# Performance work log

Hardware: AMD Instinct MI355X
Metric: run time of the kernel (lower is better)

The kernel has to match this reference:

```python
import jax, jax.numpy as jnp
import numpy as np

# constants from __init__ defaults
K_WINNERS = 5
GAIN_UP = 1.8
MIN_GAIN = 0.5
MAX_GAIN = 2.5
THETA = 1.0

B, T = 512, 8192


def setup_inputs() -> dict:
    key = jax.random.key(0)
    k1, k2, k3 = jax.random.split(key, 3)
    amp = jax.random.uniform(k1, (B, T), jnp.float32)
    pitch = jax.random.uniform(k2, (B, T), jnp.float32)
    boundary = jax.random.uniform(k3, (B, T), jnp.float32)
    decay = jnp.array([0.7, 0.7, 0.7], jnp.float32)    # buffer 'decay'
    weights = jnp.array([1.0, 1.0, 1.0], jnp.float32)  # buffer 'weights'
    return {"amp": amp, "pitch": pitch, "boundary": boundary,
            "decay": decay, "weights": weights}


def reference(amp, pitch, boundary, decay, weights):
    # Stack the 3 channels so one scan handles all LIF neurons: xs [3, B, T]
    xs = jnp.stack([amp, pitch, boundary], axis=0)
    d = decay[:, None]  # [3, 1] broadcast over batch

    def step(v, x_t):          # v, x_t: [3, B]
        v = d * v + x_t
        s = (v >= THETA).astype(v.dtype)
        return v - s * THETA, s

    v0 = jnp.zeros((3, B), xs.dtype)
    _, spikes = jax.lax.scan(step, v0, jnp.moveaxis(xs, 2, 0))  # spikes [T, 3, B]

    # salience = w_amp*s_amp + w_pitch*s_pitch + w_bound*s_bound -> [B, T]
    sal = jnp.einsum('c,tcb->bt', weights, spikes)
    # smoothing == 0 -> conv branch skipped (matches default init)
    sal = sal / (jnp.max(sal, axis=1, keepdims=True) + 1e-6)

    topk_vals, topk_idx = jax.lax.top_k(sal, K_WINNERS)  # [B, K]
    avg_winner = topk_vals.mean(axis=1)                  # [B]
    mu_scalar = MIN_GAIN + (MAX_GAIN - MIN_GAIN) * jnp.tanh(GAIN_UP * avg_winner)
    return mu_scalar, sal, topk_idx
```

## Files before the change

kernel.cpp:

```cpp
#include <hip/hip_runtime.h>
#include <cstdint>
#include <cstddef>

#define BB 512
#define TT 8192
#define TW 256
#define KWIN 5

static __device__ __forceinline__ float fract_f(float x) {
#if __has_builtin(__builtin_amdgcn_fractf)
    return __builtin_amdgcn_fractf(x);
#else
    return x - floorf(x);
#endif
}

__global__ __launch_bounds__(64, 2)
void lif_scan_kernel(const float* __restrict__ amp,
                     const float* __restrict__ pitch,
                     const float* __restrict__ boundary,
                     const float* __restrict__ decay,
                     float* __restrict__ out)
{
    const int blk = blockIdx.x;
    const int c   = blk >> 9;
    const int b   = blk & 511;
    const int l   = threadIdx.x;
    const float* __restrict__ src =
        (c == 0 ? amp : (c == 1 ? pitch : boundary)) + (size_t)b * TT;
    const float dv = decay[c];

    const float4* __restrict__ w4 = reinterpret_cast<const float4*>(src) + 32 * l;
    float4 W[32];
#pragma unroll
    for (int i = 0; i < 32; ++i) W[i] = w4[i];

    float v = 0.0f;

    const bool z = (l == 0);
#define WSTEP(xx)                                               \
    {                                                           \
        float xw = __shfl_up((xx), 1);                          \
        if (z) xw = 0.0f;                                       \
        float t2 = __fadd_rn(__fmul_rn(dv, v), xw);             \
        v = fract_f(t2);                                        \
    }
#pragma unroll
    for (int i = 0; i < 32; ++i) {
        WSTEP(W[i].x) WSTEP(W[i].y) WSTEP(W[i].z) WSTEP(W[i].w)
    }
#undef WSTEP

    uint32_t w[4];
    float bs;
#define KSTEP(xx)                                               \
    {                                                           \
        float t2 = __fadd_rn(__fmul_rn(dv, v), (xx));           \
        float nv = fract_f(t2);                                 \
        bs = __builtin_fmaf(2.0f, bs, t2 - nv);                 \
        v = nv;                                                 \
    }
#pragma unroll
    for (int q = 0; q < 4; ++q) {
        bs = 0.0f;
#pragma unroll
        for (int i = 8 * q; i < 8 * q + 4; ++i) {
            KSTEP(W[i].x) KSTEP(W[i].y) KSTEP(W[i].z) KSTEP(W[i].w)
        }
        const uint32_t hi = (uint32_t)bs;
        bs = 0.0f;
#pragma unroll
        for (int i = 8 * q + 4; i < 8 * q + 8; ++i) {
            KSTEP(W[i].x) KSTEP(W[i].y) KSTEP(W[i].z) KSTEP(W[i].w)
        }
        w[q] = (hi << 16) | (uint32_t)bs;
    }
#undef KSTEP

    uint32_t* wout = reinterpret_cast<uint32_t*>(out + 512 + (size_t)b * TT)
                   + c * TW;
    *reinterpret_cast<uint4*>(wout + 4 * l) = make_uint4(w[0], w[1], w[2], w[3]);
}

__global__ __launch_bounds__(256, 2)
void salience_topk_kernel(const float* __restrict__ weights,
                          float* __restrict__ out)
{
    const int b = blockIdx.x;
    const int tid = threadIdx.x;

    __shared__ uint32_t words[3 * TW];
    __shared__ uint32_t spres[4];
    __shared__ float ntab[8];
    __shared__ uint32_t htab[8];
    __shared__ unsigned long long red[4];
    __shared__ unsigned long long wins;

    float* sal_out = out + 512 + (size_t)b * TT;
    const uint32_t* wsrc = reinterpret_cast<const uint32_t*>(sal_out);

    words[tid]       = wsrc[tid];
    words[tid + 256] = wsrc[tid + 256];
    words[tid + 512] = wsrc[tid + 512];

    const float w0 = weights[0], w1 = weights[1], w2 = weights[2];
    __syncthreads();

    uint32_t pres = 0;
#pragma unroll
    for (int j = 0; j < 8; ++j) {
        const int t0 = 4 * tid + 1024 * j;
        const int wi = t0 >> 5;
        const uint32_t wa = words[wi], wp = words[TW + wi], wq = words[2 * TW + wi];
#pragma unroll
        for (int k = 0; k < 4; ++k) {
            const int sh = 31 - ((t0 & 31) + k);
            const uint32_t idx = ((wa >> sh) & 1u)
                               | (((wp >> sh) & 1u) << 1)
                               | (((wq >> sh) & 1u) << 2);
            pres |= (1u << idx);
        }
    }
#pragma unroll
    for (int off = 32; off; off >>= 1)
        pres |= __shfl_down(pres, off);
    if ((tid & 63) == 0) spres[tid >> 6] = pres;
    __syncthreads();

    if (tid < 8) {
        const uint32_t p = spres[0] | spres[1] | spres[2] | spres[3];
        float s0 = (float)(tid & 1), s1 = (float)((tid >> 1) & 1), s2 = (float)(tid >> 2);
        float tv = __fadd_rn(__fadd_rn(__fmul_rn(w0, s0), __fmul_rn(w1, s1)),
                             __fmul_rn(w2, s2));
        float m = ((p >> tid) & 1u) ? tv : -INFINITY;
        m = fmaxf(m, __shfl_xor(m, 1));
        m = fmaxf(m, __shfl_xor(m, 2));
        m = fmaxf(m, __shfl_xor(m, 4));
        const float denom = __fadd_rn(m, 1e-6f);
        float nv = tv / denom;
        ntab[tid] = nv;
        uint32_t ub = __float_as_uint(nv);
        htab[tid] = (ub & 0x80000000u) ? ~ub : (ub | 0x80000000u);
    }
    __syncthreads();

    unsigned long long t5[5] = {0ull, 0ull, 0ull, 0ull, 0ull};
#pragma unroll
    for (int j = 0; j < 8; ++j) {
        const int t0 = 4 * tid + 1024 * j;
        const int wi = t0 >> 5;
        const uint32_t wa = words[wi], wp = words[TW + wi], wq = words[2 * TW + wi];
        float4 q;
        float* qp = &q.x;
#pragma unroll
        for (int k = 0; k < 4; ++k) {
            const int sh = 31 - ((t0 & 31) + k);
            const uint32_t idx = ((wa >> sh) & 1u)
                               | (((wp >> sh) & 1u) << 1)
                               | (((wq >> sh) & 1u) << 2);
            qp[k] = ntab[idx];
            unsigned long long key = ((unsigned long long)htab[idx] << 32)
                                   | (unsigned long long)(uint32_t)(TT - 1 - (t0 + k));
            if (key > t5[4]) {
#pragma unroll
                for (int i = 0; i < 5; ++i) {
                    bool g = key > t5[i];
                    unsigned long long o = t5[i];
                    t5[i] = g ? key : o;
                    key   = g ? o : key;
                }
            }
        }
        *reinterpret_cast<float4*>(sal_out + t0) = q;
    }

    float vsum = 0.0f;
    for (int r = 0; r < KWIN; ++r) {
        unsigned long long cand = t5[0];
#pragma unroll
        for (int off = 32; off; off >>= 1) {
            unsigned long long o = __shfl_down(cand, off);
            if (o > cand) cand = o;
        }
        __syncthreads();
        if ((tid & 63) == 0) red[tid >> 6] = cand;
        __syncthreads();
        if (tid == 0) {
            unsigned long long m = red[0];
            if (red[1] > m) m = red[1];
            if (red[2] > m) m = red[2];
            if (red[3] > m) m = red[3];
            wins = m;
        }
        __syncthreads();
        const unsigned long long w = wins;
        if (t5[0] == w) {
            t5[0] = t5[1]; t5[1] = t5[2]; t5[2] = t5[3]; t5[3] = t5[4]; t5[4] = 0ull;
        }
        if (tid == 0) {
            uint32_t hi = (uint32_t)(w >> 32);
            uint32_t fb = (hi & 0x80000000u) ? (hi & 0x7FFFFFFFu) : ~hi;
            vsum += __uint_as_float(fb);
            out[512 + (size_t)BB * TT + (size_t)b * KWIN + r] =
                (float)(int)(TT - 1 - (uint32_t)(w & 0xFFFFFFFFull));
        }
    }

    if (tid == 0) {
        out[b] = 0.5f + 2.0f * tanhf(1.8f * (vsum / 5.0f));
    }
}

extern "C" void kernel_launch(void* const* d_in, const int* in_sizes, int n_in,
                              void* d_out, int out_size, void* d_ws, size_t ws_size,
                              hipStream_t stream) {
    const float* amp      = (const float*)d_in[0];
    const float* pitch    = (const float*)d_in[1];
    const float* boundary = (const float*)d_in[2];
    const float* decay    = (const float*)d_in[3];
    const float* weights  = (const float*)d_in[4];
    float* out = (float*)d_out;

    lif_scan_kernel<<<3 * BB, 64, 0, stream>>>(amp, pitch, boundary, decay, out);
    salience_topk_kernel<<<BB, 256, 0, stream>>>(weights, out);
}
```

Before: 114.6 us.

## Fuse LIF scan and salience top-k into one kernel via shared-memory bitmasks

Merges the two kernels into one launch. Three of the four waves in each 256-thread block run the per-channel LIF scans and write the spike bitmasks straight into shared memory, so the global round trip through the output buffer and the second launch go away. The cost is that the fourth wave sits idle during the scan. The block now uses 128 float4 registers per scan wave under a 256-thread launch bound, and there are only 512 blocks where the scan stage used to have 1536 blocks, so occupancy and latency hiding may drop.

```diff
diff --git a/kernel.cpp b/kernel.cpp
--- a/kernel.cpp
+++ b/kernel.cpp
@@ -15,79 +15,18 @@
 #endif
 }
 
-__global__ __launch_bounds__(64, 2)
-void lif_scan_kernel(const float* __restrict__ amp,
-                     const float* __restrict__ pitch,
-                     const float* __restrict__ boundary,
-                     const float* __restrict__ decay,
-                     float* __restrict__ out)
+__global__ __launch_bounds__(256, 2)
+void fused_spike_topk_kernel(const float* __restrict__ amp,
+                             const float* __restrict__ pitch,
+                             const float* __restrict__ boundary,
+                             const float* __restrict__ decay,
+                             const float* __restrict__ weights,
+                             float* __restrict__ out)
 {
-    const int blk = blockIdx.x;
-    const int c   = blk >> 9;
-    const int b   = blk & 511;
-    const int l   = threadIdx.x;
-    const float* __restrict__ src =
-        (c == 0 ? amp : (c == 1 ? pitch : boundary)) + (size_t)b * TT;
-    const float dv = decay[c];
-
-    const float4* __restrict__ w4 = reinterpret_cast<const float4*>(src) + 32 * l;
-    float4 W[32];
-#pragma unroll
-    for (int i = 0; i < 32; ++i) W[i] = w4[i];
-
-    float v = 0.0f;
-
-    const bool z = (l == 0);
-#define WSTEP(xx)                                               \
-    {                                                           \
-        float xw = __shfl_up((xx), 1);                          \
-        if (z) xw = 0.0f;                                       \
-        float t2 = __fadd_rn(__fmul_rn(dv, v), xw);             \
-        v = fract_f(t2);                                        \
-    }
-#pragma unroll
-    for (int i = 0; i < 32; ++i) {
-        WSTEP(W[i].x) WSTEP(W[i].y) WSTEP(W[i].z) WSTEP(W[i].w)
-    }
-#undef WSTEP
-
-    uint32_t w[4];
-    float bs;
-#define KSTEP(xx)                                               \
-    {                                                           \
-        float t2 = __fadd_rn(__fmul_rn(dv, v), (xx));           \
-        float nv = fract_f(t2);                                 \
-        bs = __builtin_fmaf(2.0f, bs, t2 - nv);                 \
-        v = nv;                                                 \
-    }
-#pragma unroll
-    for (int q = 0; q < 4; ++q) {
-        bs = 0.0f;
-#pragma unroll
-        for (int i = 8 * q; i < 8 * q + 4; ++i) {
-            KSTEP(W[i].x) KSTEP(W[i].y) KSTEP(W[i].z) KSTEP(W[i].w)
-        }
-        const uint32_t hi = (uint32_t)bs;
-        bs = 0.0f;
-#pragma unroll
-        for (int i = 8 * q + 4; i < 8 * q + 8; ++i) {
-            KSTEP(W[i].x) KSTEP(W[i].y) KSTEP(W[i].z) KSTEP(W[i].w)
-        }
-        w[q] = (hi << 16) | (uint32_t)bs;
-    }
-#undef KSTEP
-
-    uint32_t* wout = reinterpret_cast<uint32_t*>(out + 512 + (size_t)b * TT)
-                   + c * TW;
-    *reinterpret_cast<uint4*>(wout + 4 * l) = make_uint4(w[0], w[1], w[2], w[3]);
-}
-
-__global__ __launch_bounds__(256, 2)
-void salience_topk_kernel(const float* __restrict__ weights,
-                          float* __restrict__ out)
-{
-    const int b = blockIdx.x;
-    const int tid = threadIdx.x;
+    const int b    = blockIdx.x;
+    const int tid  = threadIdx.x;
+    const int wave = tid >> 6;
+    const int l    = tid & 63;
 
     __shared__ uint32_t words[3 * TW];
     __shared__ uint32_t spres[4];
@@ -96,12 +35,63 @@
     __shared__ unsigned long long red[4];
     __shared__ unsigned long long wins;
 
-    float* sal_out = out + 512 + (size_t)b * TT;
-    const uint32_t* wsrc = reinterpret_cast<const uint32_t*>(sal_out);
-
-    words[tid]       = wsrc[tid];
-    words[tid + 256] = wsrc[tid + 256];
-    words[tid + 512] = wsrc[tid + 512];
+    if (wave < 3) {
+        const int c = wave;
+        const float* __restrict__ src =
+            (c == 0 ? amp : (c == 1 ? pitch : boundary)) + (size_t)b * TT;
+        const float dv = decay[c];
+
+        const float4* __restrict__ w4 =
+            reinterpret_cast<const float4*>(src) + 32 * l;
+        float4 W[32];
+#pragma unroll
+        for (int i = 0; i < 32; ++i) W[i] = w4[i];
+
+        float v = 0.0f;
+
+        const bool z = (l == 0);
+#define WSTEP(xx)                                               \
+        {                                                       \
+            float xw = __shfl_up((xx), 1);                      \
+            if (z) xw = 0.0f;                                   \
+            float t2 = __fadd_rn(__fmul_rn(dv, v), xw);         \
+            v = fract_f(t2);                                    \
+        }
+#pragma unroll
+        for (int i = 0; i < 32; ++i) {
+            WSTEP(W[i].x) WSTEP(W[i].y) WSTEP(W[i].z) WSTEP(W[i].w)
+        }
+#undef WSTEP
+
+        uint32_t w[4];
+        float bs;
+#define KSTEP(xx)                                               \
+        {                                                       \
+            float t2 = __fadd_rn(__fmul_rn(dv, v), (xx));       \
+            float nv = fract_f(t2);                             \
+            bs = __builtin_fmaf(2.0f, bs, t2 - nv);             \
+            v = nv;                                             \
+        }
+#pragma unroll
+        for (int q = 0; q < 4; ++q) {
+            bs = 0.0f;
+#pragma unroll
+            for (int i = 8 * q; i < 8 * q + 4; ++i) {
+                KSTEP(W[i].x) KSTEP(W[i].y) KSTEP(W[i].z) KSTEP(W[i].w)
+            }
+            const uint32_t hi = (uint32_t)bs;
+            bs = 0.0f;
+#pragma unroll
+            for (int i = 8 * q + 4; i < 8 * q + 8; ++i) {
+                KSTEP(W[i].x) KSTEP(W[i].y) KSTEP(W[i].z) KSTEP(W[i].w)
+            }
+            w[q] = (hi << 16) | (uint32_t)bs;
+        }
+#undef KSTEP
+
+        *reinterpret_cast<uint4*>(&words[c * TW + 4 * l]) =
+            make_uint4(w[0], w[1], w[2], w[3]);
+    }
 
     const float w0 = weights[0], w1 = weights[1], w2 = weights[2];
     __syncthreads();
@@ -144,6 +134,7 @@
     }
     __syncthreads();
 
+    float* sal_out = out + 512 + (size_t)b * TT;
     unsigned long long t5[5] = {0ull, 0ull, 0ull, 0ull, 0ull};
 #pragma unroll
     for (int j = 0; j < 8; ++j) {
@@ -221,6 +212,6 @@
     const float* weights  = (const float*)d_in[4];
     float* out = (float*)d_out;
 
-    lif_scan_kernel<<<3 * BB, 64, 0, stream>>>(amp, pitch, boundary, decay, out);
-    salience_topk_kernel<<<BB, 256, 0, stream>>>(weights, out);
+    fused_spike_topk_kernel<<<BB, 256, 0, stream>>>(amp, pitch, boundary,
+                                                    decay, weights, out);
 }
```

Result: faster. 111.8 us (-2.5%).
